# Kernel tuning notes

Measured on AMD Instinct MI355X. Metric: run time of the kernel, lower is better.

The kernel has to match this reference:

```python
import jax, jax.numpy as jnp
import numpy as np

N_NODES = 50000
N_EDGES = 1600000
F_IN = 128
HID = 128
N_GRAPHS = 64
N_CLASSES = 2
EPS = 1e-5


def _gcn_conv(x, W, b, src, dst, n_nodes):
    # x: [N, Fin] -> [N, Fout]; PyG GCNConv: add self-loops, sym-normalize, aggregate at dst
    h = x @ W  # [N, Fout]
    deg = jax.ops.segment_sum(jnp.ones_like(dst, dtype=h.dtype), dst, num_segments=n_nodes)
    dinv = jnp.where(deg > 0, jax.lax.rsqrt(jnp.maximum(deg, 1.0)), 0.0)
    norm = dinv[src] * dinv[dst]  # [E]
    msgs = h[src] * norm[:, None]  # [E, Fout] gather
    out = jax.ops.segment_sum(msgs, dst, num_segments=n_nodes)  # scatter-add
    return out + b


def _batch_norm(x, gamma, beta):
    # training-style batch statistics over node dim
    mu = jnp.mean(x, axis=0)
    var = jnp.var(x, axis=0)
    return (x - mu) * jax.lax.rsqrt(var + EPS) * gamma + beta


def setup_inputs() -> dict:
    key = jax.random.key(0)
    ks = jax.random.split(key, 16)
    x = jax.random.normal(ks[0], (N_NODES, F_IN), dtype=jnp.float32)
    edge_index = jax.random.randint(ks[1], (2, N_EDGES), 0, N_NODES, dtype=jnp.int32)
    batch = jnp.sort(jax.random.randint(ks[2], (N_NODES,), 0, N_GRAPHS, dtype=jnp.int32))
    s = 0.05
    params = {
        "W1": jax.random.normal(ks[3], (F_IN, HID), jnp.float32) * s,
        "b1": jnp.zeros((HID,), jnp.float32),
        "g1": jnp.ones((HID,), jnp.float32),
        "be1": jnp.zeros((HID,), jnp.float32),
        "W2": jax.random.normal(ks[4], (HID, HID), jnp.float32) * s,
        "b2": jnp.zeros((HID,), jnp.float32),
        "g2": jnp.ones((HID,), jnp.float32),
        "be2": jnp.zeros((HID,), jnp.float32),
        "W3": jax.random.normal(ks[5], (HID, HID), jnp.float32) * s,
        "b3": jnp.zeros((HID,), jnp.float32),
        "g3": jnp.ones((HID,), jnp.float32),
        "be3": jnp.zeros((HID,), jnp.float32),
        "Wc1": jax.random.normal(ks[6], (HID, HID // 2), jnp.float32) * s,
        "bc1": jnp.zeros((HID // 2,), jnp.float32),
        "Wc2": jax.random.normal(ks[7], (HID // 2, N_CLASSES), jnp.float32) * s,
        "bc2": jnp.zeros((N_CLASSES,), jnp.float32),
    }
    return {"x": x, "edge_index": edge_index, "batch": batch, **params}


def reference(x, edge_index, batch, W1, b1, g1, be1, W2, b2, g2, be2, W3, b3, g3, be3, Wc1, bc1, Wc2, bc2):
    n = x.shape[0]
    self_loops = jnp.arange(n, dtype=edge_index.dtype)
    src = jnp.concatenate([edge_index[0], self_loops])
    dst = jnp.concatenate([edge_index[1], self_loops])

    h = _gcn_conv(x, W1, b1, src, dst, n)
    h = jax.nn.relu(_batch_norm(h, g1, be1))
    h = _gcn_conv(h, W2, b2, src, dst, n)
    h = jax.nn.relu(_batch_norm(h, g2, be2))
    h = _gcn_conv(h, W3, b3, src, dst, n)
    h = _batch_norm(h, g3, be3)

    # global mean pool over graphs
    sums = jax.ops.segment_sum(h, batch, num_segments=N_GRAPHS)
    cnt = jax.ops.segment_sum(jnp.ones((n,), h.dtype), batch, num_segments=N_GRAPHS)
    gemb = sums / jnp.maximum(cnt, 1.0)[:, None]  # [G, HID]

    z = jax.nn.relu(gemb @ Wc1 + bc1)
    logits = z @ Wc2 + bc2  # [G, C]
    return logits
```

## Files before the change

kernel.cpp:

```cpp
#include <hip/hip_runtime.h>
#include <hip/hip_bf16.h>
#include <cstdint>

static inline size_t align_up(size_t x, size_t a) { return (x + a - 1) & ~(a - 1); }

#define ELLW 96
#define NG 256
#define QPAD 16
#define PARTMAX 224

typedef __attribute__((ext_vector_type(8))) short short8v;
typedef __attribute__((ext_vector_type(4))) float f32x4;

__device__ inline unsigned bf16_rne(float f) {
  unsigned u = __float_as_uint(f);
  return (u + 0x7fffu + ((u >> 16) & 1u)) >> 16;
}
__device__ inline float blo(unsigned u) { return __uint_as_float(u << 16); }
__device__ inline float bhi(unsigned u) { return __uint_as_float(u & 0xffff0000u); }

union FragU { uint4 q; short8v v; unsigned short us[8]; };


__global__ __launch_bounds__(256) void part_kernel(const int* __restrict__ src, const int* __restrict__ dst,
                                                   int* __restrict__ qtail, unsigned* __restrict__ queue,
                                                   int qcap, int E, int part) {
  __shared__ int lcnt[NG], lbase[NG], lcur[NG];
  int per = (E + gridDim.x - 1) / gridDim.x;
  int e0 = blockIdx.x * per;
  int e1 = min(e0 + per, E);
  for (int t = threadIdx.x; t < NG; t += 256) { lcnt[t] = 0; lcur[t] = 0; }
  __syncthreads();
  for (int i = e0 + threadIdx.x; i < e1; i += 256) {
    int d = dst[i];
    atomicAdd(&lcnt[d / part], 1);
  }
  __syncthreads();
  for (int t = threadIdx.x; t < NG; t += 256)
    lbase[t] = atomicAdd(&qtail[t * QPAD], lcnt[t]);
  __syncthreads();
  for (int i = e0 + threadIdx.x; i < e1; i += 256) {
    int d = dst[i];
    int s = src[i];
    int g = d / part;
    int pos = lbase[g] + atomicAdd(&lcur[g], 1);
    if (pos < qcap) queue[(size_t)g * qcap + pos] = ((unsigned)d << 16) | (unsigned)s;
  }
}


__global__ __launch_bounds__(256) void fill_kernel(const unsigned* __restrict__ queue,
                                                   const int* __restrict__ qtail, int qcap,
                                                   int* __restrict__ cnt, unsigned short* __restrict__ ell,
                                                   int n, int part) {
  __shared__ int lcur[PARTMAX];
  int g = blockIdx.x;
  int lo = g * part;
  if (lo >= n) return;
  int nn = min(lo + part, n) - lo;
  for (int t = threadIdx.x; t < nn; t += 256) lcur[t] = 0;
  __syncthreads();
  int len = min(qtail[g * QPAD], qcap);
  const unsigned* q = queue + (size_t)g * qcap;
  for (int i = threadIdx.x; i < len; i += 256) {
    unsigned e = q[i];
    int d = (int)(e >> 16);
    int s = (int)(e & 0xffffu);
    int pos = atomicAdd(&lcur[d - lo], 1);
    if (pos < ELLW) ell[(size_t)d * ELLW + pos] = (unsigned short)s;
  }
  __syncthreads();
  for (int t = threadIdx.x; t < nn; t += 256) cnt[lo + t] = lcur[t];
}


__global__ __launch_bounds__(256) void wconv_kernel(const float* __restrict__ W1, const float* __restrict__ W2,
                                                    const float* __restrict__ W3, unsigned short* __restrict__ Wf) {
  const float* W = (blockIdx.x == 0) ? W1 : (blockIdx.x == 1) ? W2 : W3;
  uint4* o = (uint4*)(Wf + (size_t)blockIdx.x * 16384);
  for (int e = threadIdx.x; e < 2048; e += 256) {
    int t = e >> 8, s = (e >> 6) & 3, l = e & 63;
    int kb = s * 32 + ((l >> 4) << 3);
    int col = t * 16 + (l & 15);
    FragU f;
    #pragma unroll
    for (int j = 0; j < 8; ++j) f.us[j] = (unsigned short)bf16_rne(W[(size_t)(kb + j) * 128 + col]);
    o[e] = f.q;
  }
}


__global__ __launch_bounds__(256) void gemm_kernel(const float* __restrict__ inf, const unsigned short* __restrict__ inb,
                                                   const unsigned short* __restrict__ Wf,
                                                   const float* __restrict__ stat, const float* __restrict__ gam,
                                                   const float* __restrict__ bet, const int* __restrict__ cnt,
                                                   unsigned short* __restrict__ hp, int n, int mode, float inv_n) {
  __shared__ float Ls[64][132];
  __shared__ float scs[128], shs[128];
  int tid = threadIdx.x;
  int row0 = blockIdx.x * 64;

  if (mode) {
    if (tid < 128) {
      float mu = stat[tid] * inv_n;
      float var = stat[128 + tid] * inv_n - mu * mu;
      float rstd = rsqrtf(var + 1e-5f);
      float s = gam[tid] * rstd;
      scs[tid] = s;
      shs[tid] = fmaf(-mu, s, bet[tid]);
    }
    __syncthreads();
  }

  int l = tid & 63;
  int w = tid >> 6;
  int r0 = row0 + w * 16;
  int rowA = r0 + (l & 15);
  int kgrp = (l >> 4) * 8;

  f32x4 acc[8];
  #pragma unroll
  for (int t = 0; t < 8; ++t) acc[t] = (f32x4){0.f, 0.f, 0.f, 0.f};

  const uint4* Wf4 = (const uint4*)Wf;

  #pragma unroll
  for (int s = 0; s < 4; ++s) {
    int kb = s * 32 + kgrp;
    FragU a;
    if (rowA < n) {
      if (mode) {
        FragU ua;
        ua.q = ((const uint4*)inb)[(size_t)rowA * 16 + (kb >> 3)];
        #pragma unroll
        for (int j = 0; j < 2; ++j) {}
        float xv;
        unsigned uu;
        uu = ua.q.x; xv = fmaxf(fmaf(blo(uu), scs[kb + 0], shs[kb + 0]), 0.f); a.us[0] = (unsigned short)bf16_rne(xv);
                     xv = fmaxf(fmaf(bhi(uu), scs[kb + 1], shs[kb + 1]), 0.f); a.us[1] = (unsigned short)bf16_rne(xv);
        uu = ua.q.y; xv = fmaxf(fmaf(blo(uu), scs[kb + 2], shs[kb + 2]), 0.f); a.us[2] = (unsigned short)bf16_rne(xv);
                     xv = fmaxf(fmaf(bhi(uu), scs[kb + 3], shs[kb + 3]), 0.f); a.us[3] = (unsigned short)bf16_rne(xv);
        uu = ua.q.z; xv = fmaxf(fmaf(blo(uu), scs[kb + 4], shs[kb + 4]), 0.f); a.us[4] = (unsigned short)bf16_rne(xv);
                     xv = fmaxf(fmaf(bhi(uu), scs[kb + 5], shs[kb + 5]), 0.f); a.us[5] = (unsigned short)bf16_rne(xv);
        uu = ua.q.w; xv = fmaxf(fmaf(blo(uu), scs[kb + 6], shs[kb + 6]), 0.f); a.us[6] = (unsigned short)bf16_rne(xv);
                     xv = fmaxf(fmaf(bhi(uu), scs[kb + 7], shs[kb + 7]), 0.f); a.us[7] = (unsigned short)bf16_rne(xv);
      } else {
        const float* ap = inf + (size_t)rowA * 128 + kb;
        float4 f0 = *(const float4*)(ap);
        float4 f1 = *(const float4*)(ap + 4);
        a.us[0] = (unsigned short)bf16_rne(f0.x); a.us[1] = (unsigned short)bf16_rne(f0.y);
        a.us[2] = (unsigned short)bf16_rne(f0.z); a.us[3] = (unsigned short)bf16_rne(f0.w);
        a.us[4] = (unsigned short)bf16_rne(f1.x); a.us[5] = (unsigned short)bf16_rne(f1.y);
        a.us[6] = (unsigned short)bf16_rne(f1.z); a.us[7] = (unsigned short)bf16_rne(f1.w);
      }
    } else {
      a.q = make_uint4(0, 0, 0, 0);
    }
    #pragma unroll
    for (int t = 0; t < 8; ++t) {
      FragU b;
      b.q = Wf4[(t * 4 + s) * 64 + l];
      acc[t] = __builtin_amdgcn_mfma_f32_16x16x32_bf16(a.v, b.v, acc[t], 0, 0, 0);
    }
  }

  #pragma unroll
  for (int t = 0; t < 8; ++t) {
    int col = t * 16 + (l & 15);
    int rb = w * 16 + (l >> 4) * 4;
    #pragma unroll
    for (int i = 0; i < 4; ++i) Ls[rb + i][col] = acc[t][i];
  }
  __syncthreads();

  int tx = tid & 15;
  int ty = tid >> 4;
  #pragma unroll
  for (int i = 0; i < 4; ++i) {
    int ro = ty + 16 * i;
    int row = row0 + ro;
    if (row < n) {
      float dv = rsqrtf((float)(cnt[row] + 1));
      const float* lp = &Ls[ro][tx * 8];
      unsigned o[4];
      #pragma unroll
      for (int c = 0; c < 4; ++c) {
        unsigned lo = bf16_rne(lp[2 * c] * dv);
        unsigned hi = bf16_rne(lp[2 * c + 1] * dv);
        o[c] = lo | (hi << 16);
      }
      *(uint4*)(hp + (size_t)row * 128 + tx * 8) = make_uint4(o[0], o[1], o[2], o[3]);
    }
  }
}


__global__ __launch_bounds__(256) void agg_kernel(const unsigned short* __restrict__ hp,
                                                  const unsigned short* __restrict__ ell,
                                                  const int* __restrict__ cnt,
                                                  const float* __restrict__ bias, unsigned short* __restrict__ out,
                                                  int n) {
  int wave = threadIdx.x >> 6;
  int lane = threadIdx.x & 63;
  int node = blockIdx.x * 16 + wave * 4 + (lane >> 4);
  if (node >= n) return;
  int sub = lane & 15;

  const uint4* hp4 = (const uint4*)hp;
  uint4 u = hp4[(size_t)node * 16 + sub];
  float a0 = blo(u.x), a1 = bhi(u.x), a2 = blo(u.y), a3 = bhi(u.y);
  float a4 = blo(u.z), a5 = bhi(u.z), a6 = blo(u.w), a7 = bhi(u.w);

  int c = cnt[node];
  int deg = min(c, ELLW);
  const unsigned short* row = ell + (size_t)node * ELLW;
  int e = 0;
  for (; e + 3 < deg; e += 4) {
    ushort4 idx = *(const ushort4*)(row + e);
    uint4 u0 = hp4[(size_t)idx.x * 16 + sub];
    uint4 u1 = hp4[(size_t)idx.y * 16 + sub];
    uint4 u2 = hp4[(size_t)idx.z * 16 + sub];
    uint4 u3 = hp4[(size_t)idx.w * 16 + sub];
    a0 += blo(u0.x) + blo(u1.x) + blo(u2.x) + blo(u3.x);
    a1 += bhi(u0.x) + bhi(u1.x) + bhi(u2.x) + bhi(u3.x);
    a2 += blo(u0.y) + blo(u1.y) + blo(u2.y) + blo(u3.y);
    a3 += bhi(u0.y) + bhi(u1.y) + bhi(u2.y) + bhi(u3.y);
    a4 += blo(u0.z) + blo(u1.z) + blo(u2.z) + blo(u3.z);
    a5 += bhi(u0.z) + bhi(u1.z) + bhi(u2.z) + bhi(u3.z);
    a6 += blo(u0.w) + blo(u1.w) + blo(u2.w) + blo(u3.w);
    a7 += bhi(u0.w) + bhi(u1.w) + bhi(u2.w) + bhi(u3.w);
  }
  for (; e < deg; ++e) {
    uint4 uu = hp4[(size_t)row[e] * 16 + sub];
    a0 += blo(uu.x); a1 += bhi(uu.x); a2 += blo(uu.y); a3 += bhi(uu.y);
    a4 += blo(uu.z); a5 += bhi(uu.z); a6 += blo(uu.w); a7 += bhi(uu.w);
  }

  float dv = rsqrtf((float)(c + 1));
  int f0 = sub * 8;
  float v0 = fmaf(a0, dv, bias[f0]);
  float v1 = fmaf(a1, dv, bias[f0 + 1]);
  float v2 = fmaf(a2, dv, bias[f0 + 2]);
  float v3 = fmaf(a3, dv, bias[f0 + 3]);
  float v4 = fmaf(a4, dv, bias[f0 + 4]);
  float v5 = fmaf(a5, dv, bias[f0 + 5]);
  float v6 = fmaf(a6, dv, bias[f0 + 6]);
  float v7 = fmaf(a7, dv, bias[f0 + 7]);
  unsigned o0 = bf16_rne(v0) | (bf16_rne(v1) << 16);
  unsigned o1 = bf16_rne(v2) | (bf16_rne(v3) << 16);
  unsigned o2 = bf16_rne(v4) | (bf16_rne(v5) << 16);
  unsigned o3 = bf16_rne(v6) | (bf16_rne(v7) << 16);
  *(uint4*)(out + (size_t)node * 128 + f0) = make_uint4(o0, o1, o2, o3);
}


__global__ __launch_bounds__(256) void stats_kernel(const unsigned short* __restrict__ X, float* __restrict__ stat, int n) {
  int u = threadIdx.x & 63;
  int h = threadIdx.x >> 6;
  int base = blockIdx.x * 256;
  int end = min(base + 256, n);
  const unsigned* Xu = (const unsigned*)X;
  float s0 = 0.f, q0 = 0.f, s1 = 0.f, q1 = 0.f;
  for (int r = base + h; r < end; r += 4) {
    unsigned v = Xu[(size_t)r * 64 + u];
    float x0 = blo(v), x1 = bhi(v);
    s0 += x0; q0 += x0 * x0;
    s1 += x1; q1 += x1 * x1;
  }
  __shared__ float L0[256], L1[256], L2[256], L3[256];
  L0[threadIdx.x] = s0; L1[threadIdx.x] = q0; L2[threadIdx.x] = s1; L3[threadIdx.x] = q1;
  __syncthreads();
  if (h == 0) {
    #pragma unroll
    for (int hh = 1; hh < 4; ++hh) {
      s0 += L0[u + 64 * hh]; q0 += L1[u + 64 * hh];
      s1 += L2[u + 64 * hh]; q1 += L3[u + 64 * hh];
    }
    atomicAdd(&stat[2 * u], s0);
    atomicAdd(&stat[2 * u + 1], s1);
    atomicAdd(&stat[128 + 2 * u], q0);
    atomicAdd(&stat[128 + 2 * u + 1], q1);
  }
}


__global__ __launch_bounds__(128) void pool_stats(const unsigned short* __restrict__ X, const int* __restrict__ batch,
                                                  float* __restrict__ gsum, int* __restrict__ gcnt,
                                                  float* __restrict__ stat, int n) {
  int base = blockIdx.x * 64;
  if (base >= n) return;
  int f = threadIdx.x;
  int end = min(base + 64, n);
  int curg = batch[base];
  float acc = 0.f, s = 0.f, q = 0.f;
  int c = 0;
  for (int r = base; r < end; ++r) {
    float v = __uint_as_float((unsigned)X[(size_t)r * 128 + f] << 16);
    s += v; q += v * v;
    int g = batch[r];
    if (g != curg) {
      atomicAdd(&gsum[(size_t)curg * 128 + f], acc);
      if (f == 0) atomicAdd(&gcnt[curg], c);
      acc = 0.f; c = 0; curg = g;
    }
    acc += v;
    c++;
  }
  atomicAdd(&gsum[(size_t)curg * 128 + f], acc);
  if (f == 0) atomicAdd(&gcnt[curg], c);
  atomicAdd(&stat[f], s);
  atomicAdd(&stat[128 + f], q);
}


__global__ __launch_bounds__(64) void head_kernel(const float* __restrict__ gsum, const int* __restrict__ gcnt,
                                                  const float* __restrict__ stat, const float* __restrict__ g3,
                                                  const float* __restrict__ be3,
                                                  const float* __restrict__ Wc1, const float* __restrict__ bc1,
                                                  const float* __restrict__ Wc2, const float* __restrict__ bc2,
                                                  float* __restrict__ out, float inv_n) {
  __shared__ float ge[128];
  __shared__ float z[64];
  int gb = blockIdx.x, j = threadIdx.x;
  float c = fmaxf((float)gcnt[gb], 1.0f);
  #pragma unroll
  for (int h = 0; h < 2; ++h) {
    int f = j + h * 64;
    float mu = stat[f] * inv_n;
    float var = stat[128 + f] * inv_n - mu * mu;
    float rstd = rsqrtf(var + 1e-5f);
    float sc = g3[f] * rstd;
    float sh = fmaf(-mu, sc, be3[f]);
    ge[f] = fmaf(gsum[(size_t)gb * 128 + f] / c, sc, sh);
  }
  __syncthreads();
  float a = bc1[j];
  #pragma unroll 8
  for (int k = 0; k < 128; ++k) a = fmaf(ge[k], Wc1[k * 64 + j], a);
  z[j] = fmaxf(a, 0.f);
  __syncthreads();
  if (j < 2) {
    float l = bc2[j];
    #pragma unroll 8
    for (int k = 0; k < 64; ++k) l = fmaf(z[k], Wc2[k * 2 + j], l);
    out[gb * 2 + j] = l;
  }
}


extern "C" void kernel_launch(void* const* d_in, const int* in_sizes, int n_in,
                              void* d_out, int out_size, void* d_ws, size_t ws_size,
                              hipStream_t stream) {
  const float* x    = (const float*)d_in[0];
  const int*   ei   = (const int*)d_in[1];
  const int*   batch= (const int*)d_in[2];
  const float* W1   = (const float*)d_in[3];
  const float* b1   = (const float*)d_in[4];
  const float* g1   = (const float*)d_in[5];
  const float* be1  = (const float*)d_in[6];
  const float* W2   = (const float*)d_in[7];
  const float* b2   = (const float*)d_in[8];
  const float* g2   = (const float*)d_in[9];
  const float* be2  = (const float*)d_in[10];
  const float* W3   = (const float*)d_in[11];
  const float* b3   = (const float*)d_in[12];
  const float* g3   = (const float*)d_in[13];
  const float* be3  = (const float*)d_in[14];
  const float* Wc1  = (const float*)d_in[15];
  const float* bc1  = (const float*)d_in[16];
  const float* Wc2  = (const float*)d_in[17];
  const float* bc2  = (const float*)d_in[18];

  int N = in_sizes[0] / 128;
  int E = in_sizes[1] / 2;
  int G = out_size / 2;
  int part = (N + NG - 1) / NG;
  int qcap = E / NG + 1024;

  char* p = (char*)d_ws;
  int* cnt    = (int*)p;   p += align_up((size_t)N * 4, 256);
  int* qtail  = (int*)p;   p += align_up((size_t)NG * QPAD * 4, 256);
  float* stats= (float*)p; p += align_up(3 * 256 * 4, 256);
  float* gsum = (float*)p; p += align_up((size_t)G * 128 * 4, 256);
  int* gcnt   = (int*)p;   p += align_up((size_t)G * 4, 256);
  size_t zero_bytes = (size_t)(p - (char*)d_ws);
  unsigned* queue = (unsigned*)p; p += align_up((size_t)NG * qcap * 4, 256);
  unsigned short* ell  = (unsigned short*)p; p += align_up((size_t)N * ELLW * 2, 256);
  unsigned short* hp   = (unsigned short*)p; p += align_up((size_t)N * 128 * 2, 256);
  unsigned short* bufb = (unsigned short*)p; p += align_up((size_t)N * 128 * 2, 256);
  unsigned short* Wf   = (unsigned short*)p; p += align_up((size_t)3 * 16384 * 2, 256);

  hipMemsetAsync(d_ws, 0, zero_bytes, stream);

  wconv_kernel<<<3, 256, 0, stream>>>(W1, W2, W3, Wf);
  part_kernel<<<512, 256, 0, stream>>>(ei, ei + E, qtail, queue, qcap, E, part);
  fill_kernel<<<NG, 256, 0, stream>>>(queue, qtail, qcap, cnt, ell, N, part);

  int gblocks = (N + 63) / 64;
  int ablocks = (N + 15) / 16;
  int sblocks = (N + 255) / 256;
  int pblocks = (N + 63) / 64;
  float inv_n = 1.0f / (float)N;

  gemm_kernel<<<gblocks, 256, 0, stream>>>(x, bufb, Wf, stats, g1, be1, cnt, hp, N, 0, inv_n);
  agg_kernel<<<ablocks, 256, 0, stream>>>(hp, ell, cnt, b1, bufb, N);
  stats_kernel<<<sblocks, 256, 0, stream>>>(bufb, stats + 0, N);

  gemm_kernel<<<gblocks, 256, 0, stream>>>(x, bufb, Wf + 16384, stats + 0, g1, be1, cnt, hp, N, 1, inv_n);
  agg_kernel<<<ablocks, 256, 0, stream>>>(hp, ell, cnt, b2, bufb, N);
  stats_kernel<<<sblocks, 256, 0, stream>>>(bufb, stats + 256, N);

  gemm_kernel<<<gblocks, 256, 0, stream>>>(x, bufb, Wf + 32768, stats + 256, g2, be2, cnt, hp, N, 1, inv_n);
  agg_kernel<<<ablocks, 256, 0, stream>>>(hp, ell, cnt, b3, bufb, N);

  pool_stats<<<pblocks, 128, 0, stream>>>(bufb, batch, gsum, gcnt, stats + 512, N);
  head_kernel<<<G, 64, 0, stream>>>(gsum, gcnt, stats + 512, g3, be3, Wc1, bc1, Wc2, bc2, (float*)d_out, inv_n);
}
```

Baseline: 340.6 us.

## Sub-bin edge partition by source octant and fold weight conversion into partition kernel

Edges are now partitioned into 256×8 bins keyed by destination group and source octant, so fill_kernel writes each node's ELL row with sources grouped by source range. This makes ELL neighbor lists roughly sorted by source, which should improve gather locality in the aggregation kernels. The weight-conversion kernel is merged into the partition kernel as three extra blocks, saving one launch. The cost is eight times more global queue atomics and bins, smaller per-bin capacity with a risk of overflow, and extra syncs in fill.

New measurement: 344.9 us. No clear change (+1.3%).

```diff
diff --git a/kernel.cpp b/kernel.cpp
--- a/kernel.cpp
+++ b/kernel.cpp
@@ -6,6 +6,8 @@
 
 #define ELLW 96
 #define NG 256
+#define NOCT 8
+#define NBIN (NG * NOCT)
 #define QPAD 16
 #define PARTMAX 224
 
@@ -24,33 +26,56 @@
 
 __global__ __launch_bounds__(256) void part_kernel(const int* __restrict__ src, const int* __restrict__ dst,
                                                    int* __restrict__ qtail, unsigned* __restrict__ queue,
-                                                   int qcap, int E, int part) {
-  __shared__ int lcnt[NG], lbase[NG], lcur[NG];
-  int per = (E + gridDim.x - 1) / gridDim.x;
+                                                   int qcap8, int E, int part, int octpart,
+                                                   const float* __restrict__ W1, const float* __restrict__ W2,
+                                                   const float* __restrict__ W3, unsigned short* __restrict__ Wf,
+                                                   int pblocks) {
+  __shared__ int lcnt[NBIN], lbase[NBIN], lcur[NBIN];
+
+  if (blockIdx.x >= pblocks) {
+    int wi = blockIdx.x - pblocks;
+    const float* W = (wi == 0) ? W1 : (wi == 1) ? W2 : W3;
+    uint4* o = (uint4*)(Wf + (size_t)wi * 16384);
+    for (int e = threadIdx.x; e < 2048; e += 256) {
+      int t = e >> 8, s = (e >> 6) & 3, l = e & 63;
+      int kb = s * 32 + ((l >> 4) << 3);
+      int col = t * 16 + (l & 15);
+      FragU f;
+      #pragma unroll
+      for (int j = 0; j < 8; ++j) f.us[j] = (unsigned short)bf16_rne(W[(size_t)(kb + j) * 128 + col]);
+      o[e] = f.q;
+    }
+    return;
+  }
+
+  int per = (E + pblocks - 1) / pblocks;
   int e0 = blockIdx.x * per;
   int e1 = min(e0 + per, E);
-  for (int t = threadIdx.x; t < NG; t += 256) { lcnt[t] = 0; lcur[t] = 0; }
-  __syncthreads();
-  for (int i = e0 + threadIdx.x; i < e1; i += 256) {
-    int d = dst[i];
-    atomicAdd(&lcnt[d / part], 1);
-  }
-  __syncthreads();
-  for (int t = threadIdx.x; t < NG; t += 256)
-    lbase[t] = atomicAdd(&qtail[t * QPAD], lcnt[t]);
+  for (int t = threadIdx.x; t < NBIN; t += 256) { lcnt[t] = 0; lcur[t] = 0; }
   __syncthreads();
   for (int i = e0 + threadIdx.x; i < e1; i += 256) {
     int d = dst[i];
     int s = src[i];
-    int g = d / part;
-    int pos = lbase[g] + atomicAdd(&lcur[g], 1);
-    if (pos < qcap) queue[(size_t)g * qcap + pos] = ((unsigned)d << 16) | (unsigned)s;
+    atomicAdd(&lcnt[(d / part) * NOCT + (s / octpart)], 1);
+  }
+  __syncthreads();
+  for (int t = threadIdx.x; t < NBIN; t += 256) {
+    int c = lcnt[t];
+    lbase[t] = c ? atomicAdd(&qtail[t * QPAD], c) : 0;
+  }
+  __syncthreads();
+  for (int i = e0 + threadIdx.x; i < e1; i += 256) {
+    int d = dst[i];
+    int s = src[i];
+    int bin = (d / part) * NOCT + (s / octpart);
+    int pos = lbase[bin] + atomicAdd(&lcur[bin], 1);
+    if (pos < qcap8) queue[(size_t)bin * qcap8 + pos] = ((unsigned)d << 16) | (unsigned)s;
   }
 }
 
 
 __global__ __launch_bounds__(256) void fill_kernel(const unsigned* __restrict__ queue,
-                                                   const int* __restrict__ qtail, int qcap,
+                                                   const int* __restrict__ qtail, int qcap8,
                                                    int* __restrict__ cnt, unsigned short* __restrict__ ell,
                                                    int n, int part) {
   __shared__ int lcur[PARTMAX];
@@ -60,33 +85,21 @@
   int nn = min(lo + part, n) - lo;
   for (int t = threadIdx.x; t < nn; t += 256) lcur[t] = 0;
   __syncthreads();
-  int len = min(qtail[g * QPAD], qcap);
-  const unsigned* q = queue + (size_t)g * qcap;
-  for (int i = threadIdx.x; i < len; i += 256) {
-    unsigned e = q[i];
-    int d = (int)(e >> 16);
-    int s = (int)(e & 0xffffu);
-    int pos = atomicAdd(&lcur[d - lo], 1);
-    if (pos < ELLW) ell[(size_t)d * ELLW + pos] = (unsigned short)s;
-  }
-  __syncthreads();
+  #pragma unroll
+  for (int o = 0; o < NOCT; ++o) {
+    int bin = g * NOCT + o;
+    int len = min(qtail[bin * QPAD], qcap8);
+    const unsigned* q = queue + (size_t)bin * qcap8;
+    for (int i = threadIdx.x; i < len; i += 256) {
+      unsigned e = q[i];
+      int d = (int)(e >> 16);
+      int s = (int)(e & 0xffffu);
+      int pos = atomicAdd(&lcur[d - lo], 1);
+      if (pos < ELLW) ell[(size_t)d * ELLW + pos] = (unsigned short)s;
+    }
+    __syncthreads();
+  }
   for (int t = threadIdx.x; t < nn; t += 256) cnt[lo + t] = lcur[t];
-}
-
-
-__global__ __launch_bounds__(256) void wconv_kernel(const float* __restrict__ W1, const float* __restrict__ W2,
-                                                    const float* __restrict__ W3, unsigned short* __restrict__ Wf) {
-  const float* W = (blockIdx.x == 0) ? W1 : (blockIdx.x == 1) ? W2 : W3;
-  uint4* o = (uint4*)(Wf + (size_t)blockIdx.x * 16384);
-  for (int e = threadIdx.x; e < 2048; e += 256) {
-    int t = e >> 8, s = (e >> 6) & 3, l = e & 63;
-    int kb = s * 32 + ((l >> 4) << 3);
-    int col = t * 16 + (l & 15);
-    FragU f;
-    #pragma unroll
-    for (int j = 0; j < 8; ++j) f.us[j] = (unsigned short)bf16_rne(W[(size_t)(kb + j) * 128 + col]);
-    o[e] = f.q;
-  }
 }
 
 
@@ -132,8 +145,6 @@
       if (mode) {
         FragU ua;
         ua.q = ((const uint4*)inb)[(size_t)rowA * 16 + (kb >> 3)];
-        #pragma unroll
-        for (int j = 0; j < 2; ++j) {}
         float xv;
         unsigned uu;
         uu = ua.q.x; xv = fmaxf(fmaf(blo(uu), scs[kb + 0], shs[kb + 0]), 0.f); a.us[0] = (unsigned short)bf16_rne(xv);
@@ -375,16 +386,18 @@
   int E = in_sizes[1] / 2;
   int G = out_size / 2;
   int part = (N + NG - 1) / NG;
-  int qcap = E / NG + 1024;
+  int octpart = (N + NOCT - 1) / NOCT;
+  int qcap8 = E / NBIN + 512;
+  int pblocks = 512;
 
   char* p = (char*)d_ws;
   int* cnt    = (int*)p;   p += align_up((size_t)N * 4, 256);
-  int* qtail  = (int*)p;   p += align_up((size_t)NG * QPAD * 4, 256);
+  int* qtail  = (int*)p;   p += align_up((size_t)NBIN * QPAD * 4, 256);
   float* stats= (float*)p; p += align_up(3 * 256 * 4, 256);
   float* gsum = (float*)p; p += align_up((size_t)G * 128 * 4, 256);
   int* gcnt   = (int*)p;   p += align_up((size_t)G * 4, 256);
   size_t zero_bytes = (size_t)(p - (char*)d_ws);
-  unsigned* queue = (unsigned*)p; p += align_up((size_t)NG * qcap * 4, 256);
+  unsigned* queue = (unsigned*)p; p += align_up((size_t)NBIN * qcap8 * 4, 256);
   unsigned short* ell  = (unsigned short*)p; p += align_up((size_t)N * ELLW * 2, 256);
   unsigned short* hp   = (unsigned short*)p; p += align_up((size_t)N * 128 * 2, 256);
   unsigned short* bufb = (unsigned short*)p; p += align_up((size_t)N * 128 * 2, 256);
@@ -392,14 +405,14 @@
 
   hipMemsetAsync(d_ws, 0, zero_bytes, stream);
 
-  wconv_kernel<<<3, 256, 0, stream>>>(W1, W2, W3, Wf);
-  part_kernel<<<512, 256, 0, stream>>>(ei, ei + E, qtail, queue, qcap, E, part);
-  fill_kernel<<<NG, 256, 0, stream>>>(queue, qtail, qcap, cnt, ell, N, part);
+  part_kernel<<<pblocks + 3, 256, 0, stream>>>(ei, ei + E, qtail, queue, qcap8, E, part, octpart,
+                                               W1, W2, W3, Wf, pblocks);
+  fill_kernel<<<NG, 256, 0, stream>>>(queue, qtail, qcap8, cnt, ell, N, part);
 
   int gblocks = (N + 63) / 64;
   int ablocks = (N + 15) / 16;
   int sblocks = (N + 255) / 256;
-  int pblocks = (N + 63) / 64;
+  int pblocks2 = (N + 63) / 64;
   float inv_n = 1.0f / (float)N;
 
   gemm_kernel<<<gblocks, 256, 0, stream>>>(x, bufb, Wf, stats, g1, be1, cnt, hp, N, 0, inv_n);
@@ -413,6 +426,6 @@
   gemm_kernel<<<gblocks, 256, 0, stream>>>(x, bufb, Wf + 32768, stats + 256, g2, be2, cnt, hp, N, 1, inv_n);
   agg_kernel<<<ablocks, 256, 0, stream>>>(hp, ell, cnt, b3, bufb, N);
 
-  pool_stats<<<pblocks, 128, 0, stream>>>(bufb, batch, gsum, gcnt, stats + 512, N);
+  pool_stats<<<pblocks2, 128, 0, stream>>>(bufb, batch, gsum, gcnt, stats + 512, N);
   head_kernel<<<G, 64, 0, stream>>>(gsum, gcnt, stats + 512, g3, be3, Wc1, bc1, Wc2, bc2, (float*)d_out, inv_n);
 }
```

## Order ELL neighbors by source octant and fold weight conversion into partition kernel

Applied to the files above, without the earlier changes.

The fill kernel now copies each partition's edge queue into shared memory, then makes eight passes over it. Each pass inserts only edges whose source falls in one eighth of the node range, so each ELL row lists its neighbors grouped by source region. This aims to improve cache locality of the feature gathers in the aggregation kernels. Separately, the bf16 weight-fragment conversion moves into three extra blocks of the partition kernel, which removes one kernel launch. The cost is a 32 KB shared staging buffer, which could fail if a partition queue ever exceeds QSTAGE, plus eight scans of the queue per block.

Result: faster. 331.4 us (-2.7%).

```diff
diff --git a/kernel.cpp b/kernel.cpp
--- a/kernel.cpp
+++ b/kernel.cpp
@@ -6,8 +6,10 @@
 
 #define ELLW 96
 #define NG 256
+#define NOCT 8
 #define QPAD 16
 #define PARTMAX 224
+#define QSTAGE 8192
 
 typedef __attribute__((ext_vector_type(8))) short short8v;
 typedef __attribute__((ext_vector_type(4))) float f32x4;
@@ -24,9 +26,29 @@
 
 __global__ __launch_bounds__(256) void part_kernel(const int* __restrict__ src, const int* __restrict__ dst,
                                                    int* __restrict__ qtail, unsigned* __restrict__ queue,
-                                                   int qcap, int E, int part) {
+                                                   int qcap, int E, int part,
+                                                   const float* __restrict__ W1, const float* __restrict__ W2,
+                                                   const float* __restrict__ W3, unsigned short* __restrict__ Wf,
+                                                   int pblocks) {
   __shared__ int lcnt[NG], lbase[NG], lcur[NG];
-  int per = (E + gridDim.x - 1) / gridDim.x;
+
+  if (blockIdx.x >= pblocks) {
+    int wi = blockIdx.x - pblocks;
+    const float* W = (wi == 0) ? W1 : (wi == 1) ? W2 : W3;
+    uint4* o = (uint4*)(Wf + (size_t)wi * 16384);
+    for (int e = threadIdx.x; e < 2048; e += 256) {
+      int t = e >> 8, s = (e >> 6) & 3, l = e & 63;
+      int kb = s * 32 + ((l >> 4) << 3);
+      int col = t * 16 + (l & 15);
+      FragU f;
+      #pragma unroll
+      for (int j = 0; j < 8; ++j) f.us[j] = (unsigned short)bf16_rne(W[(size_t)(kb + j) * 128 + col]);
+      o[e] = f.q;
+    }
+    return;
+  }
+
+  int per = (E + pblocks - 1) / pblocks;
   int e0 = blockIdx.x * per;
   int e1 = min(e0 + per, E);
   for (int t = threadIdx.x; t < NG; t += 256) { lcnt[t] = 0; lcur[t] = 0; }
@@ -52,41 +74,33 @@
 __global__ __launch_bounds__(256) void fill_kernel(const unsigned* __restrict__ queue,
                                                    const int* __restrict__ qtail, int qcap,
                                                    int* __restrict__ cnt, unsigned short* __restrict__ ell,
-                                                   int n, int part) {
+                                                   int n, int part, int octpart) {
   __shared__ int lcur[PARTMAX];
+  __shared__ unsigned qs[QSTAGE];
   int g = blockIdx.x;
   int lo = g * part;
   if (lo >= n) return;
   int nn = min(lo + part, n) - lo;
   for (int t = threadIdx.x; t < nn; t += 256) lcur[t] = 0;
-  __syncthreads();
   int len = min(qtail[g * QPAD], qcap);
   const unsigned* q = queue + (size_t)g * qcap;
-  for (int i = threadIdx.x; i < len; i += 256) {
-    unsigned e = q[i];
-    int d = (int)(e >> 16);
-    int s = (int)(e & 0xffffu);
-    int pos = atomicAdd(&lcur[d - lo], 1);
-    if (pos < ELLW) ell[(size_t)d * ELLW + pos] = (unsigned short)s;
-  }
-  __syncthreads();
+  for (int i = threadIdx.x; i < len; i += 256) qs[i] = q[i];
+  __syncthreads();
+  for (int o = 0; o < NOCT; ++o) {
+    int slo = o * octpart;
+    int shi = slo + octpart;
+    for (int i = threadIdx.x; i < len; i += 256) {
+      unsigned e = qs[i];
+      int s = (int)(e & 0xffffu);
+      if (s >= slo && s < shi) {
+        int d = (int)(e >> 16);
+        int pos = atomicAdd(&lcur[d - lo], 1);
+        if (pos < ELLW) ell[(size_t)d * ELLW + pos] = (unsigned short)s;
+      }
+    }
+    __syncthreads();
+  }
   for (int t = threadIdx.x; t < nn; t += 256) cnt[lo + t] = lcur[t];
-}
-
-
-__global__ __launch_bounds__(256) void wconv_kernel(const float* __restrict__ W1, const float* __restrict__ W2,
-                                                    const float* __restrict__ W3, unsigned short* __restrict__ Wf) {
-  const float* W = (blockIdx.x == 0) ? W1 : (blockIdx.x == 1) ? W2 : W3;
-  uint4* o = (uint4*)(Wf + (size_t)blockIdx.x * 16384);
-  for (int e = threadIdx.x; e < 2048; e += 256) {
-    int t = e >> 8, s = (e >> 6) & 3, l = e & 63;
-    int kb = s * 32 + ((l >> 4) << 3);
-    int col = t * 16 + (l & 15);
-    FragU f;
-    #pragma unroll
-    for (int j = 0; j < 8; ++j) f.us[j] = (unsigned short)bf16_rne(W[(size_t)(kb + j) * 128 + col]);
-    o[e] = f.q;
-  }
 }
 
 
@@ -132,8 +146,6 @@
       if (mode) {
         FragU ua;
         ua.q = ((const uint4*)inb)[(size_t)rowA * 16 + (kb >> 3)];
-        #pragma unroll
-        for (int j = 0; j < 2; ++j) {}
         float xv;
         unsigned uu;
         uu = ua.q.x; xv = fmaxf(fmaf(blo(uu), scs[kb + 0], shs[kb + 0]), 0.f); a.us[0] = (unsigned short)bf16_rne(xv);
@@ -375,7 +387,9 @@
   int E = in_sizes[1] / 2;
   int G = out_size / 2;
   int part = (N + NG - 1) / NG;
+  int octpart = (N + NOCT - 1) / NOCT;
   int qcap = E / NG + 1024;
+  int pblocks = 512;
 
   char* p = (char*)d_ws;
   int* cnt    = (int*)p;   p += align_up((size_t)N * 4, 256);
@@ -392,14 +406,14 @@
 
   hipMemsetAsync(d_ws, 0, zero_bytes, stream);
 
-  wconv_kernel<<<3, 256, 0, stream>>>(W1, W2, W3, Wf);
-  part_kernel<<<512, 256, 0, stream>>>(ei, ei + E, qtail, queue, qcap, E, part);
-  fill_kernel<<<NG, 256, 0, stream>>>(queue, qtail, qcap, cnt, ell, N, part);
+  part_kernel<<<pblocks + 3, 256, 0, stream>>>(ei, ei + E, qtail, queue, qcap, E, part,
+                                               W1, W2, W3, Wf, pblocks);
+  fill_kernel<<<NG, 256, 0, stream>>>(queue, qtail, qcap, cnt, ell, N, part, octpart);
 
   int gblocks = (N + 63) / 64;
   int ablocks = (N + 15) / 16;
   int sblocks = (N + 255) / 256;
-  int pblocks = (N + 63) / 64;
+  int pblocks2 = (N + 63) / 64;
   float inv_n = 1.0f / (float)N;
 
   gemm_kernel<<<gblocks, 256, 0, stream>>>(x, bufb, Wf, stats, g1, be1, cnt, hp, N, 0, inv_n);
@@ -413,6 +427,6 @@
   gemm_kernel<<<gblocks, 256, 0, stream>>>(x, bufb, Wf + 32768, stats + 256, g2, be2, cnt, hp, N, 1, inv_n);
   agg_kernel<<<ablocks, 256, 0, stream>>>(hp, ell, cnt, b3, bufb, N);
 
-  pool_stats<<<pblocks, 128, 0, stream>>>(bufb, batch, gsum, gcnt, stats + 512, N);
+  pool_stats<<<pblocks2, 128, 0, stream>>>(bufb, batch, gsum, gcnt, stats + 512, N);
   head_kernel<<<G, 64, 0, stream>>>(gsum, gcnt, stats + 512, g3, be3, Wc1, bc1, Wc2, bc2, (float*)d_out, inv_n);
 }
```
